# Optimization experiments

Hardware: AMD Instinct MI355X
Metric: run time of the kernel (lower is better)

The kernel has to match this reference:

```python
import jax, jax.numpy as jnp
import numpy as np

B, T, D, P, ALPHA, PR = 4, 4096, 1024, 512, 4, 64


def setup_inputs() -> dict:
    key = jax.random.key(0)
    ks = jax.random.split(key, 9)
    g = lambda k, shape, scale: jax.random.normal(k, shape, jnp.float32) * scale
    return {
        "x": jax.random.normal(ks[0], (B, T, D), jnp.float32),
        "W_toP": g(ks[1], (D, P), D ** -0.5),
        "W_U": g(ks[2], (D, P, ALPHA), D ** -0.5),
        "W_F": g(ks[3], (D, P), D ** -0.5),
        "W_V": g(ks[4], (P, ALPHA), 1.0),
        "W_lam": g(ks[5], (P, PR), P ** -0.5),
        "B_mat": g(ks[6], (P, PR), P ** -0.5),
        "C_mat": g(ks[7], (PR, P), PR ** -0.5),
        "W_fromP": g(ks[8], (P, D), P ** -0.5),
    }


def reference(x, W_toP, W_U, W_F, W_V, W_lam, B_mat, C_mat, W_fromP):
    # dense pre-path: (B,T,D)->(B,T,P)
    pre = jnp.einsum('btd,dp->btp', x, W_toP)
    # CeptaEmbedding dense pathway: multi-factor projection U, gates F, weighted Y
    U = jnp.einsum('btd,dpa->btpa', x, W_U)            # (B,T,P,alpha)
    Fg = jax.nn.sigmoid(jnp.einsum('btd,dp->btp', x, W_F))  # (B,T,P) in (0,1)
    Y = U * W_V                                        # (B,T,P,alpha)
    # CeptaRouting(reduce='sum'): sum over alpha factors, plus residual pre-path
    t = Y.sum(-1) + pre                                # (B,T,P)
    # CeptaSSMLowRank: input-dependent diagonal decay in rank-PR state space
    lam = jax.nn.sigmoid(jnp.einsum('btp,pr->btr', Fg, W_lam))  # (B,T,PR)
    u_in = jnp.einsum('btp,pr->btr', t, B_mat)                  # (B,T,PR)

    def step(s, inp):
        l, u = inp
        s = l * s + u
        return s, s

    s0 = jnp.zeros((x.shape[0], PR), x.dtype)
    _, s_seq = jax.lax.scan(step, s0, (lam.transpose(1, 0, 2), u_in.transpose(1, 0, 2)))
    s_seq = s_seq.transpose(1, 0, 2)                   # (B,T,PR)
    t_tilde = t + jnp.einsum('btr,rp->btp', s_seq, C_mat)
    h = jnp.einsum('btp,pd->btd', t_tilde, W_fromP)    # dropout p=0 -> identity
    return h
```

## Files before the change

### kernel.cpp

```cpp
#include <hip/hip_runtime.h>
#include <hip/hip_bf16.h>

#define Bb 4
#define Tt 4096
#define Dd 1024
#define Pp 512
#define PRr 64
#define Mm (Bb*Tt)
#define NCH 64
#define CL  64

typedef __bf16 bf16;
typedef __bf16 bf16x8 __attribute__((ext_vector_type(8)));
typedef __bf16 bf16x4 __attribute__((ext_vector_type(4)));
typedef float f32x4 __attribute__((ext_vector_type(4)));

#define GPTR(p) (const __attribute__((address_space(1))) void*)(p)
#define LPTR(p) (__attribute__((address_space(3))) void*)(p)

__device__ __forceinline__ float sigmoidf_(float x) {
    return 1.0f / (1.0f + __expf(-x));
}


__global__ void prep_w1(const float* __restrict__ W_toP, const float* __restrict__ W_U,
                        const float* __restrict__ W_V, const float* __restrict__ W_F,
                        bf16* __restrict__ W1t) {
    int idx = blockIdx.x * 256 + threadIdx.x;
    int n = idx >> 10, k = idx & 1023;
    float v;
    if (n < Pp) {
        int p = n;
        float4 u  = *(const float4*)(W_U + ((size_t)k * Pp + p) * 4);
        float4 wv = *(const float4*)(W_V + (size_t)p * 4);
        v = W_toP[(size_t)k * Pp + p] + u.x * wv.x + u.y * wv.y + u.z * wv.z + u.w * wv.w;
    } else {
        v = W_F[(size_t)k * Pp + (n - Pp)];
    }
    W1t[idx] = (bf16)v;
}

__global__ void prep_w3(const float* __restrict__ B_mat, const float* __restrict__ W_lam,
                        bf16* __restrict__ W3t) {
    int idx = blockIdx.x * 256 + threadIdx.x;
    int n = idx >> 10, k = idx & 1023;
    float v = 0.0f;
    if (n < PRr) { if (k < Pp) v = B_mat[(size_t)k * PRr + n]; }
    else         { if (k >= Pp) v = W_lam[(size_t)(k - Pp) * PRr + (n - PRr)]; }
    W3t[idx] = (bf16)v;
}

__global__ void prep_w2(const float* __restrict__ W_fromP, const float* __restrict__ C_mat,
                        bf16* __restrict__ W2t) {
    int n = blockIdx.x;
    int k = threadIdx.x;
    float v;
    if (k < Pp) {
        v = W_fromP[(size_t)k * Dd + n];
    } else {
        int r = k - Pp;
        float acc = 0.0f;
        #pragma unroll 8
        for (int p = 0; p < Pp; p++)
            acc = fmaf(C_mat[(size_t)r * Pp + p], W_fromP[(size_t)p * Dd + n], acc);
        v = acc;
    }
    W2t[(size_t)n * 576 + k] = (bf16)v;
}

__global__ void cast_x(const float* __restrict__ x, bf16* __restrict__ xb) {
    int i = blockIdx.x * 256 + threadIdx.x;
    float4 v = ((const float4*)x)[i];
    bf16x4 o;
    o[0] = (bf16)v.x; o[1] = (bf16)v.y; o[2] = (bf16)v.z; o[3] = (bf16)v.w;
    ((bf16x4*)xb)[i] = o;
}

__global__ void scan_phase1(const float* __restrict__ UL,
                            float* __restrict__ slocal, float* __restrict__ pprod,
                            float* __restrict__ carryS, float* __restrict__ carryP) {
    int b = blockIdx.y, c = blockIdx.x, r = threadIdx.x;
    const float* ulb = UL + ((size_t)b * Tt + (size_t)c * CL) * 128;
    float* sl = slocal + ((size_t)b * Tt + (size_t)c * CL) * PRr;
    float* pp = pprod  + ((size_t)b * Tt + (size_t)c * CL) * PRr;
    float s = 0.0f, p = 1.0f;
    for (int t0 = 0; t0 < CL; t0 += 16) {
        float uv[16], lv[16];
        #pragma unroll
        for (int i = 0; i < 16; i++) {
            uv[i] = ulb[(size_t)(t0 + i) * 128 + r];
            lv[i] = ulb[(size_t)(t0 + i) * 128 + 64 + r];
        }
        #pragma unroll
        for (int i = 0; i < 16; i++) {
            s = fmaf(lv[i], s, uv[i]);
            p *= lv[i];
            sl[(size_t)(t0 + i) * PRr + r] = s;
            pp[(size_t)(t0 + i) * PRr + r] = p;
        }
    }
    int ci = b * NCH + c;
    carryS[(size_t)ci * PRr + r] = s;
    carryP[(size_t)ci * PRr + r] = p;
}

__global__ void scan_phase2(const float* __restrict__ carryS, const float* __restrict__ carryP,
                            float* __restrict__ carryIn) {
    int b = blockIdx.x, r = threadIdx.x;
    float carry = 0.0f;
    for (int c0 = 0; c0 < NCH; c0 += 16) {
        float cs[16], cp[16];
        #pragma unroll
        for (int i = 0; i < 16; i++) {
            size_t idx = ((size_t)b * NCH + c0 + i) * PRr + r;
            cs[i] = carryS[idx];
            cp[i] = carryP[idx];
        }
        #pragma unroll
        for (int i = 0; i < 16; i++) {
            carryIn[((size_t)b * NCH + c0 + i) * PRr + r] = carry;
            carry = fmaf(cp[i], carry, cs[i]);
        }
    }
}

__global__ void scan_phase3(const float* __restrict__ slocal, const float* __restrict__ pprod,
                            const float* __restrict__ carryIn, bf16* __restrict__ sb) {
    int i = blockIdx.x * 256 + threadIdx.x;
    int r = i & (PRr - 1);
    int row = i >> 6;
    int b = row >> 12;
    int t = row & (Tt - 1);
    int c = t / CL;
    float carry = carryIn[((size_t)b * NCH + c) * PRr + r];
    sb[i] = (bf16)fmaf(pprod[i], carry, slocal[i]);
}

template <int EPI>
__global__ __launch_bounds__(512, 2) void gemm256(
    const bf16* __restrict__ A0, int lda0,
    const bf16* __restrict__ A1, int lda1, int ksplit,
    const bf16* __restrict__ Bt, int ldb, int K,
    void* __restrict__ Cout, int ldc, int sigcol) {

    __shared__ bf16 As[2][256 * 64];
    __shared__ bf16 Bs[2][256 * 64];

    const int tid  = threadIdx.x;
    const int lane = tid & 63;
    const int wid  = tid >> 6;
    const int wm   = wid >> 2;
    const int wn   = wid & 3;

    const int cpx = gridDim.x >> 3;
    const int bid = blockIdx.x;
    const int swz = (bid & 7) * cpx + (bid >> 3);
    const int mBase = (swz >> 2) * 256;
    const int nBase = (swz & 3) * 256;

    const int lr  = lane & 15;
    const int q16 = (lane >> 4) * 16;

    auto srcA = [&](int kt, const bf16*& src, int& lda, int& kc) {
        if (kt < ksplit) { src = A0; lda = lda0; kc = kt; }
        else             { src = A1; lda = lda1; kc = kt - ksplit; }
    };

    auto stage = [&](const bf16* src, int lda, int kc, int rowBase, bf16* lbuf, int rd) {
        int d = rd * 8192 + tid * 16;
        int L = d ^ (((d >> 7) & 7) << 4);
        int r = L >> 7;
        int c = (L & 127) >> 1;
        const bf16* g = src + (size_t)(rowBase + r) * lda + (kc + c);
        __builtin_amdgcn_global_load_lds(GPTR(g), LPTR((char*)lbuf + d), 16, 0, 0);
    };

    auto frag = [&](const bf16* lbuf, int r, int cb) -> bf16x8 {
        int flat = r * 128 + cb;
        int phys = flat ^ (((flat >> 7) & 7) << 4);
        return *(const bf16x8*)((const char*)lbuf + phys);
    };

    const int NT = K / 64;

    {
        const bf16* sa; int la, kc; srcA(0, sa, la, kc);
        stage(sa, la, kc, mBase, As[0], 0); stage(sa, la, kc, mBase, As[0], 2);
        stage(Bt, ldb, 0, nBase, Bs[0], 0); stage(Bt, ldb, 0, nBase, Bs[0], 1);
        stage(Bt, ldb, 0, nBase, Bs[0], 2); stage(Bt, ldb, 0, nBase, Bs[0], 3);
        stage(sa, la, kc, mBase, As[0], 1); stage(sa, la, kc, mBase, As[0], 3);
    }
    asm volatile("s_waitcnt vmcnt(2)" ::: "memory");
    __builtin_amdgcn_s_barrier();

    f32x4 acc[8][4] = {};
    bf16x8 a[4], b0[4], b1[4];

    for (int t = 0; t < NT; ++t) {
        bf16* Ac = As[t & 1];       bf16* Bc = Bs[t & 1];
        bf16* An = As[(t + 1) & 1]; bf16* Bn = Bs[(t + 1) & 1];
        const bool hn = (t + 1 < NT);
        const bf16* sa = A0; int la = lda0, kc = 0;
        if (hn) srcA((t + 1) * 64, sa, la, kc);
        const int ktn = (t + 1) * 64;

        #pragma unroll
        for (int i = 0; i < 4; ++i) a[i]  = frag(Ac, wm * 128 + i * 16 + lr, q16);
        #pragma unroll
        for (int i = 0; i < 4; ++i) b0[i] = frag(Bc, wn * 64 + i * 16 + lr, q16);
        if (hn) {
            stage(sa, la, kc, mBase, An, 0); stage(sa, la, kc, mBase, An, 2);
            asm volatile("s_waitcnt vmcnt(2)" ::: "memory");
        } else {
            asm volatile("s_waitcnt vmcnt(0)" ::: "memory");
        }
        __builtin_amdgcn_s_barrier();
        __builtin_amdgcn_s_setprio(1);
        #pragma unroll
        for (int m = 0; m < 4; ++m)
            #pragma unroll
            for (int n = 0; n < 4; ++n)
                acc[m][n] = __builtin_amdgcn_mfma_f32_16x16x32_bf16(a[m], b0[n], acc[m][n], 0, 0, 0);
        __builtin_amdgcn_s_setprio(0);
        __builtin_amdgcn_s_barrier();

        #pragma unroll
        for (int i = 0; i < 4; ++i) a[i] = frag(Ac, wm * 128 + (i + 4) * 16 + lr, q16);
        if (hn) { stage(Bt, ldb, ktn, nBase, Bn, 0); stage(Bt, ldb, ktn, nBase, Bn, 1); }
        __builtin_amdgcn_s_barrier();
        __builtin_amdgcn_s_setprio(1);
        #pragma unroll
        for (int m = 0; m < 4; ++m)
            #pragma unroll
            for (int n = 0; n < 4; ++n)
                acc[m + 4][n] = __builtin_amdgcn_mfma_f32_16x16x32_bf16(a[m], b0[n], acc[m + 4][n], 0, 0, 0);
        __builtin_amdgcn_s_setprio(0);
        __builtin_amdgcn_s_barrier();

        #pragma unroll
        for (int i = 0; i < 4; ++i) a[i]  = frag(Ac, wm * 128 + i * 16 + lr, 64 + q16);
        #pragma unroll
        for (int i = 0; i < 4; ++i) b1[i] = frag(Bc, wn * 64 + i * 16 + lr, 64 + q16);
        if (hn) { stage(Bt, ldb, ktn, nBase, Bn, 2); stage(Bt, ldb, ktn, nBase, Bn, 3); }
        __builtin_amdgcn_s_barrier();
        __builtin_amdgcn_s_setprio(1);
        #pragma unroll
        for (int m = 0; m < 4; ++m)
            #pragma unroll
            for (int n = 0; n < 4; ++n)
                acc[m][n] = __builtin_amdgcn_mfma_f32_16x16x32_bf16(a[m], b1[n], acc[m][n], 0, 0, 0);
        __builtin_amdgcn_s_setprio(0);
        __builtin_amdgcn_s_barrier();

        #pragma unroll
        for (int i = 0; i < 4; ++i) a[i] = frag(Ac, wm * 128 + (i + 4) * 16 + lr, 64 + q16);
        if (hn) {
            stage(sa, la, kc, mBase, An, 1); stage(sa, la, kc, mBase, An, 3);
            asm volatile("s_waitcnt vmcnt(2)" ::: "memory");
        }
        __builtin_amdgcn_s_barrier();
        __builtin_amdgcn_s_setprio(1);
        #pragma unroll
        for (int m = 0; m < 4; ++m)
            #pragma unroll
            for (int n = 0; n < 4; ++n)
                acc[m + 4][n] = __builtin_amdgcn_mfma_f32_16x16x32_bf16(a[m], b1[n], acc[m + 4][n], 0, 0, 0);
        __builtin_amdgcn_s_setprio(0);
        __builtin_amdgcn_s_barrier();
    }

    const int lr4 = (lane >> 4) * 4;
    #pragma unroll
    for (int m = 0; m < 8; ++m) {
        #pragma unroll
        for (int n = 0; n < 4; ++n) {
            #pragma unroll
            for (int j = 0; j < 4; ++j) {
                int row = mBase + wm * 128 + m * 16 + lr4 + j;
                int col = nBase + wn * 64 + n * 16 + lr;
                float v = acc[m][n][j];
                if (EPI == 0) {
                    if (col >= sigcol) v = sigmoidf_(v);
                    ((bf16*)Cout)[(size_t)row * ldc + col] = (bf16)v;
                } else {
                    ((float*)Cout)[(size_t)row * ldc + col] = v;
                }
            }
        }
    }
}

template <int EPI>
__global__ __launch_bounds__(256) void gemm_bt(
    const bf16* __restrict__ A0, int lda0,
    const bf16* __restrict__ A1, int lda1, int ksplit,
    const bf16* __restrict__ Bt, int K,
    void* __restrict__ Cout, int ldc, int sigcol) {

    __shared__ bf16 As[128][32];
    __shared__ bf16 Bs[128][32];

    const int tid  = threadIdx.x;
    const int lane = tid & 63;
    const int wid  = tid >> 6;
    const int wr   = (wid >> 1) * 64;
    const int wc   = (wid & 1) * 64;
    const int mBase = blockIdx.x * 128;
    const int nBase = blockIdx.y * 128;

    f32x4 acc[4][4] = {};

    const int lr = lane & 15;
    const int lk = (lane >> 4) * 8;

    for (int kt = 0; kt < K; kt += 32) {
        const bf16* Asrc; int lda_; int kcol;
        if (kt < ksplit) { Asrc = A0; lda_ = lda0; kcol = kt; }
        else             { Asrc = A1; lda_ = lda1; kcol = kt - ksplit; }

        __syncthreads();
        #pragma unroll
        for (int i = 0; i < 2; i++) {
            int c = tid + i * 256;
            int row = c >> 2, k8 = (c & 3) * 8;
            const bf16* g = Asrc + (size_t)(mBase + row) * lda_ + (kcol + k8);
            __builtin_amdgcn_global_load_lds(GPTR(g), LPTR(&As[0][0] + c * 8), 16, 0, 0);
        }
        #pragma unroll
        for (int i = 0; i < 2; i++) {
            int c = tid + i * 256;
            int row = c >> 2, k8 = (c & 3) * 8;
            const bf16* g = Bt + (size_t)(nBase + row) * K + (kt + k8);
            __builtin_amdgcn_global_load_lds(GPTR(g), LPTR(&Bs[0][0] + c * 8), 16, 0, 0);
        }
        __syncthreads();

        bf16x8 af[4], bfr[4];
        #pragma unroll
        for (int m = 0; m < 4; m++) af[m]  = *(const bf16x8*)(&As[wr + m * 16 + lr][lk]);
        #pragma unroll
        for (int n = 0; n < 4; n++) bfr[n] = *(const bf16x8*)(&Bs[wc + n * 16 + lr][lk]);
        #pragma unroll
        for (int m = 0; m < 4; m++)
            #pragma unroll
            for (int n = 0; n < 4; n++)
                acc[m][n] = __builtin_amdgcn_mfma_f32_16x16x32_bf16(af[m], bfr[n], acc[m][n], 0, 0, 0);
    }

    const int lr4 = (lane >> 4) * 4;
    const int lc  = lane & 15;
    #pragma unroll
    for (int m = 0; m < 4; m++) {
        #pragma unroll
        for (int n = 0; n < 4; n++) {
            #pragma unroll
            for (int j = 0; j < 4; j++) {
                int row = mBase + wr + m * 16 + lr4 + j;
                int col = nBase + wc + n * 16 + lc;
                float v = acc[m][n][j];
                if (EPI == 1) {
                    if (col >= sigcol) v = sigmoidf_(v);
                    ((float*)Cout)[(size_t)row * ldc + col] = v;
                } else {
                    ((float*)Cout)[(size_t)row * ldc + col] = v;
                }
            }
        }
    }
}

extern "C" void kernel_launch(void* const* d_in, const int* in_sizes, int n_in,
                              void* d_out, int out_size, void* d_ws, size_t ws_size,
                              hipStream_t stream) {
    const float* x       = (const float*)d_in[0];
    const float* W_toP   = (const float*)d_in[1];
    const float* W_U     = (const float*)d_in[2];
    const float* W_F     = (const float*)d_in[3];
    const float* W_V     = (const float*)d_in[4];
    const float* W_lam   = (const float*)d_in[5];
    const float* B_mat   = (const float*)d_in[6];
    const float* C_mat   = (const float*)d_in[7];
    const float* W_fromP = (const float*)d_in[8];
    float* out = (float*)d_out;

    char* ws = (char*)d_ws;
    size_t off = 0;
    auto alloc = [&](size_t bytes) { void* p = ws + off; off = (off + bytes + 255) & ~255ULL; return p; };
    bf16*  xb  = (bf16*)alloc((size_t)Mm * Dd * 2);
    bf16*  TF  = (bf16*)alloc((size_t)Mm * 1024 * 2);
    float* UL  = (float*)alloc((size_t)Mm * 128 * 4);
    bf16*  sb  = (bf16*)alloc((size_t)Mm * PRr * 2);
    bf16*  W1t = (bf16*)alloc((size_t)1024 * 1024 * 2);
    bf16*  W3t = (bf16*)alloc((size_t)128 * 1024 * 2);
    bf16*  W2t = (bf16*)alloc((size_t)1024 * 576 * 2);
    float* slocal = (float*)alloc((size_t)Mm * PRr * 4);
    float* pprod  = (float*)alloc((size_t)Mm * PRr * 4);
    float* carryS = (float*)alloc((size_t)Bb * NCH * PRr * 4);
    float* carryP = (float*)alloc((size_t)Bb * NCH * PRr * 4);
    float* carryI = (float*)alloc((size_t)Bb * NCH * PRr * 4);

    prep_w1<<<dim3(4096), dim3(256), 0, stream>>>(W_toP, W_U, W_V, W_F, W1t);
    prep_w3<<<dim3(512),  dim3(256), 0, stream>>>(B_mat, W_lam, W3t);
    prep_w2<<<dim3(1024), dim3(576), 0, stream>>>(W_fromP, C_mat, W2t);
    cast_x <<<dim3(Mm * Dd / 4 / 256), dim3(256), 0, stream>>>(x, xb);

    gemm256<0><<<dim3((Mm / 256) * (1024 / 256)), 512, 0, stream>>>(
        xb, Dd, xb, Dd, 1 << 30, W1t, Dd, Dd, TF, 1024, Pp);

    gemm_bt<1><<<dim3(Mm / 128, 1), 256, 0, stream>>>(
        TF, 1024, TF, 1024, 1 << 30, W3t, 1024, UL, 128, PRr);

    scan_phase1<<<dim3(NCH, Bb), dim3(PRr), 0, stream>>>(UL, slocal, pprod, carryS, carryP);
    scan_phase2<<<dim3(Bb), dim3(PRr), 0, stream>>>(carryS, carryP, carryI);
    scan_phase3<<<dim3(Mm * PRr / 256), dim3(256), 0, stream>>>(slocal, pprod, carryI, sb);

    gemm256<2><<<dim3((Mm / 256) * (1024 / 256)), 512, 0, stream>>>(
        TF, 1024, sb, PRr, Pp, W2t, 576, 576, out, Dd, 1 << 30);
}
```

Baseline: 160.7 us.

## Deepen GEMM global-to-LDS prefetch to issue most of tile t+2 early

Restructures the double-buffered GEMM main loop so most of the A and B tiles for step t+2 are issued at the end of step t, writing into the buffer just consumed. Only the second half of A for step t+1 is loaded at the start of each iteration. The prologue now stages tile 0 plus most of tile 1, and the vmcnt waits are retuned to match. The goal is to hide more global-load latency behind MFMA work. In exchange there are more loads in flight and fragile wait-count and buffer-reuse ordering.

```diff
diff --git a/kernel.cpp b/kernel.cpp
--- a/kernel.cpp
+++ b/kernel.cpp
@@ -189,8 +189,16 @@
         stage(Bt, ldb, 0, nBase, Bs[0], 0); stage(Bt, ldb, 0, nBase, Bs[0], 1);
         stage(Bt, ldb, 0, nBase, Bs[0], 2); stage(Bt, ldb, 0, nBase, Bs[0], 3);
         stage(sa, la, kc, mBase, As[0], 1); stage(sa, la, kc, mBase, As[0], 3);
-    }
-    asm volatile("s_waitcnt vmcnt(2)" ::: "memory");
+        if (NT > 1) {
+            const bf16* s1; int l1, k1; srcA(64, s1, l1, k1);
+            stage(s1, l1, k1, mBase, As[1], 0); stage(s1, l1, k1, mBase, As[1], 2);
+            stage(Bt, ldb, 64, nBase, Bs[1], 0); stage(Bt, ldb, 64, nBase, Bs[1], 1);
+            stage(Bt, ldb, 64, nBase, Bs[1], 2); stage(Bt, ldb, 64, nBase, Bs[1], 3);
+            asm volatile("s_waitcnt vmcnt(8)" ::: "memory");
+        } else {
+            asm volatile("s_waitcnt vmcnt(2)" ::: "memory");
+        }
+    }
     __builtin_amdgcn_s_barrier();
 
     f32x4 acc[8][4] = {};
@@ -198,19 +206,22 @@
 
     for (int t = 0; t < NT; ++t) {
         bf16* Ac = As[t & 1];       bf16* Bc = Bs[t & 1];
-        bf16* An = As[(t + 1) & 1]; bf16* Bn = Bs[(t + 1) & 1];
-        const bool hn = (t + 1 < NT);
-        const bf16* sa = A0; int la = lda0, kc = 0;
-        if (hn) srcA((t + 1) * 64, sa, la, kc);
-        const int ktn = (t + 1) * 64;
+        bf16* An = As[(t + 1) & 1]; bf16* Bn2 = Bs[t & 1]; bf16* An2 = As[t & 1];
+        const bool hn1 = (t + 1 < NT);
+        const bool hn2 = (t + 2 < NT);
+        const bf16* sa1 = A0; int la1 = lda0, kc1 = 0;
+        if (hn1) srcA((t + 1) * 64, sa1, la1, kc1);
+        const bf16* sa2 = A0; int la2 = lda0, kc2 = 0;
+        if (hn2) srcA((t + 2) * 64, sa2, la2, kc2);
+        const int ktn2 = (t + 2) * 64;
 
         #pragma unroll
         for (int i = 0; i < 4; ++i) a[i]  = frag(Ac, wm * 128 + i * 16 + lr, q16);
         #pragma unroll
         for (int i = 0; i < 4; ++i) b0[i] = frag(Bc, wn * 64 + i * 16 + lr, q16);
-        if (hn) {
-            stage(sa, la, kc, mBase, An, 0); stage(sa, la, kc, mBase, An, 2);
-            asm volatile("s_waitcnt vmcnt(2)" ::: "memory");
+        if (hn1) {
+            stage(sa1, la1, kc1, mBase, An, 1); stage(sa1, la1, kc1, mBase, An, 3);
+            asm volatile("s_waitcnt vmcnt(8)" ::: "memory");
         } else {
             asm volatile("s_waitcnt vmcnt(0)" ::: "memory");
         }
@@ -226,7 +237,6 @@
 
         #pragma unroll
         for (int i = 0; i < 4; ++i) a[i] = frag(Ac, wm * 128 + (i + 4) * 16 + lr, q16);
-        if (hn) { stage(Bt, ldb, ktn, nBase, Bn, 0); stage(Bt, ldb, ktn, nBase, Bn, 1); }
         __builtin_amdgcn_s_barrier();
         __builtin_amdgcn_s_setprio(1);
         #pragma unroll
@@ -241,7 +251,6 @@
         for (int i = 0; i < 4; ++i) a[i]  = frag(Ac, wm * 128 + i * 16 + lr, 64 + q16);
         #pragma unroll
         for (int i = 0; i < 4; ++i) b1[i] = frag(Bc, wn * 64 + i * 16 + lr, 64 + q16);
-        if (hn) { stage(Bt, ldb, ktn, nBase, Bn, 2); stage(Bt, ldb, ktn, nBase, Bn, 3); }
         __builtin_amdgcn_s_barrier();
         __builtin_amdgcn_s_setprio(1);
         #pragma unroll
@@ -254,8 +263,12 @@
 
         #pragma unroll
         for (int i = 0; i < 4; ++i) a[i] = frag(Ac, wm * 128 + (i + 4) * 16 + lr, 64 + q16);
-        if (hn) {
-            stage(sa, la, kc, mBase, An, 1); stage(sa, la, kc, mBase, An, 3);
+        if (hn2) {
+            stage(sa2, la2, kc2, mBase, An2, 0); stage(sa2, la2, kc2, mBase, An2, 2);
+            stage(Bt, ldb, ktn2, nBase, Bn2, 0); stage(Bt, ldb, ktn2, nBase, Bn2, 1);
+            stage(Bt, ldb, ktn2, nBase, Bn2, 2); stage(Bt, ldb, ktn2, nBase, Bn2, 3);
+            asm volatile("s_waitcnt vmcnt(8)" ::: "memory");
+        } else if (hn1) {
             asm volatile("s_waitcnt vmcnt(2)" ::: "memory");
         }
         __builtin_amdgcn_s_barrier();
```

Measured after the change: 162.2 us. Within noise of the previous version (+0.9%).

## Split C·W_fromP precompute into its own kernel and shorten scan chunks

Applied to the files above, without the earlier changes.

The C_mat×W_fromP product moves out of the per-element loop in prep_w2 into a dedicated prep_cw kernel. That kernel stages a C row in shared memory and computes four outputs per thread with vector loads, which removes the serial 512-step dot products done by 64 of the 576 threads in each prep_w2 block. The scan now uses 256 chunks of length 16 instead of 64 of 64, packing four chunks per 256-thread block to expose more parallelism in phase 1. The cost is a longer serial carry pass in phase 2, which now walks 256 chunks, and one extra kernel launch.

```diff
diff --git a/kernel.cpp b/kernel.cpp
--- a/kernel.cpp
+++ b/kernel.cpp
@@ -7,8 +7,8 @@
 #define Pp 512
 #define PRr 64
 #define Mm (Bb*Tt)
-#define NCH 64
-#define CL  64
+#define NCH 256
+#define CL  16
 
 typedef __bf16 bf16;
 typedef __bf16 bf16x8 __attribute__((ext_vector_type(8)));
@@ -50,21 +50,34 @@
     W3t[idx] = (bf16)v;
 }
 
-__global__ void prep_w2(const float* __restrict__ W_fromP, const float* __restrict__ C_mat,
+__global__ void prep_cw(const float* __restrict__ C_mat, const float* __restrict__ W_fromP,
+                        float* __restrict__ CW) {
+    __shared__ float crow[Pp];
+    int r = blockIdx.x;
+    int tid = threadIdx.x;
+    crow[tid]       = C_mat[(size_t)r * Pp + tid];
+    crow[tid + 256] = C_mat[(size_t)r * Pp + tid + 256];
+    __syncthreads();
+    int n4 = tid * 4;
+    f32x4 acc = {};
+    #pragma unroll 4
+    for (int p = 0; p < Pp; ++p) {
+        float cv = crow[p];
+        f32x4 w = *(const f32x4*)(W_fromP + (size_t)p * Dd + n4);
+        acc.x = fmaf(cv, w.x, acc.x);
+        acc.y = fmaf(cv, w.y, acc.y);
+        acc.z = fmaf(cv, w.z, acc.z);
+        acc.w = fmaf(cv, w.w, acc.w);
+    }
+    *(f32x4*)(CW + (size_t)r * Dd + n4) = acc;
+}
+
+__global__ void prep_w2(const float* __restrict__ W_fromP, const float* __restrict__ CW,
                         bf16* __restrict__ W2t) {
     int n = blockIdx.x;
     int k = threadIdx.x;
-    float v;
-    if (k < Pp) {
-        v = W_fromP[(size_t)k * Dd + n];
-    } else {
-        int r = k - Pp;
-        float acc = 0.0f;
-        #pragma unroll 8
-        for (int p = 0; p < Pp; p++)
-            acc = fmaf(C_mat[(size_t)r * Pp + p], W_fromP[(size_t)p * Dd + n], acc);
-        v = acc;
-    }
+    float v = (k < Pp) ? W_fromP[(size_t)k * Dd + n]
+                       : CW[(size_t)(k - Pp) * Dd + n];
     W2t[(size_t)n * 576 + k] = (bf16)v;
 }
 
@@ -79,25 +92,25 @@
 __global__ void scan_phase1(const float* __restrict__ UL,
                             float* __restrict__ slocal, float* __restrict__ pprod,
                             float* __restrict__ carryS, float* __restrict__ carryP) {
-    int b = blockIdx.y, c = blockIdx.x, r = threadIdx.x;
+    int b = blockIdx.y;
+    int c = blockIdx.x * 4 + (threadIdx.x >> 6);
+    int r = threadIdx.x & 63;
     const float* ulb = UL + ((size_t)b * Tt + (size_t)c * CL) * 128;
     float* sl = slocal + ((size_t)b * Tt + (size_t)c * CL) * PRr;
     float* pp = pprod  + ((size_t)b * Tt + (size_t)c * CL) * PRr;
+    float uv[CL], lv[CL];
+    #pragma unroll
+    for (int i = 0; i < CL; i++) {
+        uv[i] = ulb[(size_t)i * 128 + r];
+        lv[i] = ulb[(size_t)i * 128 + 64 + r];
+    }
     float s = 0.0f, p = 1.0f;
-    for (int t0 = 0; t0 < CL; t0 += 16) {
-        float uv[16], lv[16];
-        #pragma unroll
-        for (int i = 0; i < 16; i++) {
-            uv[i] = ulb[(size_t)(t0 + i) * 128 + r];
-            lv[i] = ulb[(size_t)(t0 + i) * 128 + 64 + r];
-        }
-        #pragma unroll
-        for (int i = 0; i < 16; i++) {
-            s = fmaf(lv[i], s, uv[i]);
-            p *= lv[i];
-            sl[(size_t)(t0 + i) * PRr + r] = s;
-            pp[(size_t)(t0 + i) * PRr + r] = p;
-        }
+    #pragma unroll
+    for (int i = 0; i < CL; i++) {
+        s = fmaf(lv[i], s, uv[i]);
+        p *= lv[i];
+        sl[(size_t)i * PRr + r] = s;
+        pp[(size_t)i * PRr + r] = p;
     }
     int ci = b * NCH + c;
     carryS[(size_t)ci * PRr + r] = s;
@@ -393,6 +406,7 @@
     bf16*  W1t = (bf16*)alloc((size_t)1024 * 1024 * 2);
     bf16*  W3t = (bf16*)alloc((size_t)128 * 1024 * 2);
     bf16*  W2t = (bf16*)alloc((size_t)1024 * 576 * 2);
+    float* CW  = (float*)alloc((size_t)PRr * Dd * 4);
     float* slocal = (float*)alloc((size_t)Mm * PRr * 4);
     float* pprod  = (float*)alloc((size_t)Mm * PRr * 4);
     float* carryS = (float*)alloc((size_t)Bb * NCH * PRr * 4);
@@ -401,7 +415,8 @@
 
     prep_w1<<<dim3(4096), dim3(256), 0, stream>>>(W_toP, W_U, W_V, W_F, W1t);
     prep_w3<<<dim3(512),  dim3(256), 0, stream>>>(B_mat, W_lam, W3t);
-    prep_w2<<<dim3(1024), dim3(576), 0, stream>>>(W_fromP, C_mat, W2t);
+    prep_cw<<<dim3(PRr),  dim3(256), 0, stream>>>(C_mat, W_fromP, CW);
+    prep_w2<<<dim3(1024), dim3(576), 0, stream>>>(W_fromP, CW, W2t);
     cast_x <<<dim3(Mm * Dd / 4 / 256), dim3(256), 0, stream>>>(x, xb);
 
     gemm256<0><<<dim3((Mm / 256) * (1024 / 256)), 512, 0, stream>>>(
@@ -410,7 +425,7 @@
     gemm_bt<1><<<dim3(Mm / 128, 1), 256, 0, stream>>>(
         TF, 1024, TF, 1024, 1 << 30, W3t, 1024, UL, 128, PRr);
 
-    scan_phase1<<<dim3(NCH, Bb), dim3(PRr), 0, stream>>>(UL, slocal, pprod, carryS, carryP);
+    scan_phase1<<<dim3(NCH / 4, Bb), dim3(256), 0, stream>>>(UL, slocal, pprod, carryS, carryP);
     scan_phase2<<<dim3(Bb), dim3(PRr), 0, stream>>>(carryS, carryP, carryI);
     scan_phase3<<<dim3(Mm * PRr / 256), dim3(256), 0, stream>>>(slocal, pprod, carryI, sb);
 
```

After: 192.3 us. 19.7% more time.
